# Kernel optimization log

Hardware: AMD Instinct MI355X
Metric: run time of the kernel (lower is better)

## Reference

```python
import jax, jax.numpy as jnp
import numpy as np

BN_EPS = 1e-5

def setup_inputs() -> dict:
    key = jax.random.key(0)
    ks = jax.random.split(key, 6)
    B, C, N = 8, 256, 4096
    da = C // 4
    return {
        "x": jax.random.normal(ks[0], (B, C, N), dtype=jnp.float32),
        "Wq": jax.random.normal(ks[1], (da, C), dtype=jnp.float32) * (C ** -0.5),
        "Wk": jax.random.normal(ks[2], (da, C), dtype=jnp.float32) * (C ** -0.5),
        "Wv": jax.random.normal(ks[3], (C, C), dtype=jnp.float32) * (C ** -0.5),
        "Wp": jax.random.normal(ks[4], (C, C), dtype=jnp.float32) * (C ** -0.5),
        "bn_gamma": jnp.ones((C,), dtype=jnp.float32),
        "bn_beta": jnp.zeros((C,), dtype=jnp.float32),
        "bn_mean": jnp.zeros((C,), dtype=jnp.float32),
        "bn_var": jnp.ones((C,), dtype=jnp.float32),
    }

def reference(x, Wq, Wk, Wv, Wp, bn_gamma, bn_beta, bn_mean, bn_var):
    # x: [B, C, N]; 1x1 Conv1d == channel matmul
    q = jnp.einsum('bcn,dc->bnd', x, Wq)          # [B, N, da]
    k = jnp.einsum('bcn,dc->bdn', x, Wk)          # [B, da, N]
    v = jnp.einsum('bcn,dc->bnd', x, Wv)          # [B, N, C]
    energy = jnp.einsum('bnd,bdm->bnm', q, k)     # [B, N, N]
    # offset-attention double normalization: softmax over dim=1 (rows), then L1 over dim=-1
    attn = jax.nn.softmax(energy, axis=1)
    attn = attn / (1e-9 + attn.sum(axis=-1, keepdims=True))
    fsa = jnp.einsum('bnm,bmc->bcn', attn, v)     # [B, C, N]
    y = x - fsa
    h = jnp.einsum('bcn,dc->bdn', y, Wp)          # 1x1 conv of LBR
    # BatchNorm1d (inference-mode with running stats)
    inv = bn_gamma / jnp.sqrt(bn_var + BN_EPS)
    h = h * inv[None, :, None] + (bn_beta - bn_mean * inv)[None, :, None]
    return jax.nn.relu(h) + x
```

## Files before the change

kernel.cpp:

```cpp
#include <hip/hip_runtime.h>
#include <math.h>

#define BD 8
#define CD 256
#define ND 4096
#define DA 64

typedef __attribute__((ext_vector_type(8))) short short8v;
typedef __attribute__((ext_vector_type(4))) float float4v;

static __device__ __forceinline__ float4v mfma16(short8v a, short8v b, float4v c) {
  return __builtin_amdgcn_mfma_f32_16x16x32_bf16(a, b, c, 0, 0, 0);
}
static __device__ __forceinline__ unsigned short f2bf(float f) {
  union { float f; unsigned int u; } v; v.f = f;
  return (unsigned short)((v.u + 0x7fffu + ((v.u >> 16) & 1u)) >> 16);
}
static __device__ __forceinline__ float bf2f(unsigned short h) {
  union { unsigned int u; float f; } v; v.u = (unsigned int)h << 16;
  return v.f;
}
static __device__ __forceinline__ int sw(int row, int c8) {
  return row * 64 + (((c8) ^ (row & 7)) << 3);
}
typedef const __attribute__((address_space(1))) unsigned int g_u32;
typedef __attribute__((address_space(3))) unsigned int l_u32;
static __device__ __forceinline__ void gld16(const void* g, void* l) {
  __builtin_amdgcn_global_load_lds((g_u32*)g, (l_u32*)l, 16, 0, 0);
}

__global__ __launch_bounds__(256) void k_prep(const float* __restrict__ x,
                                              unsigned short* __restrict__ xTh,
                                              unsigned short* __restrict__ xTl) {
  const int n0 = blockIdx.x * 64, c0 = blockIdx.y * 64, b = blockIdx.z;
  __shared__ float Xs[64][68];
  const int tid = threadIdx.x;
  const int r0 = tid >> 4, col4 = (tid & 15) * 4;
#pragma unroll
  for (int j = 0; j < 4; ++j) {
    int r = r0 + j * 16;
    *(float4*)&Xs[r][col4] =
        *(const float4*)&x[((size_t)(b * CD + c0 + r)) * ND + n0 + col4];
  }
  __syncthreads();
  const int n = tid >> 2, cg = (tid & 3) * 16;
  unsigned short h[16], l[16];
#pragma unroll
  for (int j = 0; j < 16; ++j) {
    float v = Xs[cg + j][n];
    h[j] = f2bf(v);
    l[j] = f2bf(v - bf2f(h[j]));
  }
  size_t o = ((size_t)b * ND + n0 + n) * CD + c0 + cg;
#pragma unroll
  for (int j = 0; j < 4; ++j) {
    *(ushort4*)&xTh[o + j * 4] = *(ushort4*)&h[j * 4];
    *(ushort4*)&xTl[o + j * 4] = *(ushort4*)&l[j * 4];
  }
}

__global__ void k_prepW(const float* __restrict__ Wq, const float* __restrict__ Wk,
                        const float* __restrict__ Wv, const float* __restrict__ Wp,
                        unsigned short* Wch, unsigned short* Wcl,
                        unsigned short* Wph, unsigned short* Wpl) {
  int i = blockIdx.x * 256 + threadIdx.x;
  int row = i >> 6, c4 = (i & 63) * 4;
  const float* src; unsigned short *dh, *dl; int r, drow;
  if (row < 64)       { src = Wq; r = row;       dh = Wch; dl = Wcl; drow = row; }
  else if (row < 128) { src = Wk; r = row - 64;  dh = Wch; dl = Wcl; drow = row; }
  else if (row < 384) { src = Wv; r = row - 128; dh = Wch; dl = Wcl; drow = row; }
  else                { src = Wp; r = row - 384; dh = Wph; dl = Wpl; drow = row - 384; }
  float4 f = *(const float4*)&src[(size_t)r * 256 + c4];
  ushort4 hh, ll;
  hh.x = f2bf(f.x); hh.y = f2bf(f.y); hh.z = f2bf(f.z); hh.w = f2bf(f.w);
  ll.x = f2bf(f.x - bf2f(hh.x)); ll.y = f2bf(f.y - bf2f(hh.y));
  ll.z = f2bf(f.z - bf2f(hh.z)); ll.w = f2bf(f.w - bf2f(hh.w));
  *(ushort4*)&dh[(size_t)drow * 256 + c4] = hh;
  *(ushort4*)&dl[(size_t)drow * 256 + c4] = ll;
}

__global__ __launch_bounds__(512) void k_proj(
    const unsigned short* __restrict__ xTh, const unsigned short* __restrict__ xTl,
    const unsigned short* __restrict__ Wch, const unsigned short* __restrict__ Wcl,
    unsigned short* __restrict__ qh, unsigned short* __restrict__ kh,
    unsigned short* __restrict__ kl, unsigned short* __restrict__ vT) {
  const int n0 = blockIdx.x * 128, b = blockIdx.y;
  const int tid = threadIdx.x, w = tid >> 6, lane = tid & 63, lq = lane & 15,
            quad = lane >> 4;
  __shared__ __align__(16) unsigned short xs[2][2][128][40];
  float4v O[24];
#pragma unroll
  for (int t = 0; t < 24; ++t) O[t] = (float4v){0.f, 0.f, 0.f, 0.f};

  const int srow = tid >> 2, sc4 = tid & 3;
  uint4 rh, rl;
  auto load_slice = [&](int ks) {
    size_t a = ((size_t)b * ND + n0 + srow) * CD + ks * 32 + sc4 * 8;
    rh = *(const uint4*)(xTh + a);
    rl = *(const uint4*)(xTl + a);
  };
  auto write_slice = [&](int buf) {
    *(uint4*)&xs[buf][0][srow][sc4 * 8] = rh;
    *(uint4*)&xs[buf][1][srow][sc4 * 8] = rl;
  };
  load_slice(0); write_slice(0);
#pragma unroll 1
  for (int ks = 0; ks < 8; ++ks) {
    __syncthreads();
    if (ks < 7) load_slice(ks + 1);
    short8v bxh = *(const short8v*)&xs[ks & 1][0][w * 16 + lq][quad * 8];
    short8v bxl = *(const short8v*)&xs[ks & 1][1][w * 16 + lq][quad * 8];
#pragma unroll
    for (int t = 0; t < 24; ++t) {
      size_t a = (size_t)(t * 16 + lq) * CD + ks * 32 + quad * 8;
      short8v awh = *(const short8v*)(Wch + a);
      short8v awl = *(const short8v*)(Wcl + a);
      O[t] = mfma16(awh, bxh, O[t]);
      O[t] = mfma16(awl, bxh, O[t]);
      O[t] = mfma16(awh, bxl, O[t]);
    }
    if (ks < 7) write_slice((ks + 1) & 1);
  }
  const int n = n0 + w * 16 + lq;
#pragma unroll
  for (int t = 0; t < 24; ++t) {
    if (t < 4) {
      ushort4 hh;
      hh.x = f2bf(O[t][0]); hh.y = f2bf(O[t][1]);
      hh.z = f2bf(O[t][2]); hh.w = f2bf(O[t][3]);
      *(ushort4*)&qh[((size_t)b * ND + n) * DA + t * 16 + quad * 4] = hh;
    } else if (t < 8) {
      ushort4 hh, ll;
      hh.x = f2bf(O[t][0]); hh.y = f2bf(O[t][1]);
      hh.z = f2bf(O[t][2]); hh.w = f2bf(O[t][3]);
      ll.x = f2bf(O[t][0] - bf2f(hh.x)); ll.y = f2bf(O[t][1] - bf2f(hh.y));
      ll.z = f2bf(O[t][2] - bf2f(hh.z)); ll.w = f2bf(O[t][3] - bf2f(hh.w));
      size_t o = ((size_t)b * ND + n) * DA + (t - 4) * 16 + quad * 4;
      *(ushort4*)&kh[o] = hh;
      *(ushort4*)&kl[o] = ll;
    } else {
#pragma unroll
      for (int r = 0; r < 4; ++r) {
        int c = (t - 8) * 16 + quad * 4 + r;
        vT[((size_t)b * CD + c) * ND + n] = f2bf(O[t][r]);
      }
    }
  }
}

__global__ __launch_bounds__(512, 4) void k_colsum(
    const unsigned short* __restrict__ qh, const unsigned short* __restrict__ khp,
    const unsigned short* __restrict__ klp, float* __restrict__ Dp) {
  const int bid = blockIdx.x, b = bid & 7, half = (bid >> 3) & 1,
            m0 = (bid >> 4) * 128;
  const int nbase = half * 2048;
  const int tid = threadIdx.x, w = tid >> 6, lane = tid & 63, lq = lane & 15,
            quad = lane >> 4;
  const int mq = w & 3, nh = w >> 2;
  __shared__ __align__(16) unsigned short qbuf[3][4096];
  __shared__ float Cb[128];
  short8v bkh[2][2], bkl[2][2];
#pragma unroll
  for (int sub = 0; sub < 2; ++sub)
#pragma unroll
    for (int k = 0; k < 2; ++k) {
      size_t a = ((size_t)b * ND + m0 + mq * 32 + sub * 16 + lq) * DA + k * 32 + quad * 8;
      bkh[sub][k] = *(const short8v*)(khp + a);
      bkl[sub][k] = *(const short8v*)(klp + a);
    }
  const int srow = w * 8 + (lane >> 3), sck = lane & 7;
  auto stageQ = [&](int it, int qn) {
    const unsigned short* src = qh + ((size_t)b * ND + nbase + it * 64 + srow) * DA +
                                ((sck ^ (srow & 7)) << 3);
    gld16(src, &qbuf[qn][0] + (size_t)w * 512);
  };
  stageQ(0, 0);
  stageQ(1, 1);
  asm volatile("s_waitcnt vmcnt(1)\n\ts_barrier" ::: "memory");
  float cs0 = 0.f, cs1 = 0.f;
  int rc = 0, sc = 2;
#pragma unroll 1
  for (int i = 0; i < 32; ++i) {
    if (i < 30) { stageQ(i + 2, sc); sc = (sc + 1 == 3) ? 0 : sc + 1; }
#pragma unroll
    for (int s = 0; s < 2; ++s) {
      short8v ah[2];
#pragma unroll
      for (int k = 0; k < 2; ++k)
        ah[k] = *(const short8v*)&qbuf[rc][sw(nh * 32 + s * 16 + lq, k * 4 + quad)];
#pragma unroll
      for (int sub = 0; sub < 2; ++sub) {
        float4v acc = {0.f, 0.f, 0.f, 0.f};
#pragma unroll
        for (int k = 0; k < 2; ++k) {
          acc = mfma16(ah[k], bkh[sub][k], acc);
          acc = mfma16(ah[k], bkl[sub][k], acc);
        }
        float e0 = __expf(acc[0]) + __expf(acc[1]) + __expf(acc[2]) + __expf(acc[3]);
        if (sub == 0) cs0 += e0; else cs1 += e0;
      }
    }
    rc = (rc + 1 == 3) ? 0 : rc + 1;
    if (i < 30)
      asm volatile("s_waitcnt vmcnt(1) lgkmcnt(0)\n\ts_barrier" ::: "memory");
    else
      asm volatile("s_waitcnt vmcnt(0) lgkmcnt(0)\n\ts_barrier" ::: "memory");
  }
  cs0 += __shfl_down(cs0, 16); cs0 += __shfl_down(cs0, 32);
  cs1 += __shfl_down(cs1, 16); cs1 += __shfl_down(cs1, 32);
  if (nh == 0 && lane < 16) {
    Cb[mq * 32 + lane] = cs0;
    Cb[mq * 32 + 16 + lane] = cs1;
  }
  __syncthreads();
  if (nh == 1 && lane < 16) {
    float t0 = Cb[mq * 32 + lane] + cs0;
    float t1 = Cb[mq * 32 + 16 + lane] + cs1;
    size_t o = (size_t)half * (BD * ND) + (size_t)b * ND + m0 + mq * 32 + lane;
    Dp[o] = t0;
    Dp[o + 16] = t1;
  }
}

__global__ void k_rcp(const float* __restrict__ Dp, float* __restrict__ Drec) {
  int i = blockIdx.x * 256 + threadIdx.x;
  float4 a = *(const float4*)&Dp[(size_t)i * 4];
  float4 c = *(const float4*)&Dp[(size_t)(BD * ND) + (size_t)i * 4];
  float4 r;
  r.x = 1.f / (a.x + c.x); r.y = 1.f / (a.y + c.y);
  r.z = 1.f / (a.z + c.z); r.w = 1.f / (a.w + c.w);
  *(float4*)&Drec[(size_t)i * 4] = r;
}

__global__ __launch_bounds__(512, 2) void k_attn(
    const unsigned short* __restrict__ qh, const unsigned short* __restrict__ khp,
    const unsigned short* __restrict__ klp, const unsigned short* __restrict__ vT,
    const float* __restrict__ Drec, unsigned short* xhy,
    const unsigned short* __restrict__ xTl) {
  const int bid = blockIdx.x, b = bid & 7, n0 = (bid >> 3) * 128;
  const int tid = threadIdx.x, w = tid >> 6, lane = tid & 63, lq = lane & 15,
            quad = lane >> 4;
  const int nh = w & 1, mt = w >> 1;
  __shared__ __align__(16) unsigned short vbuf[3][16384];
  __shared__ __align__(16) unsigned short Pb[2][8192];
  __shared__ float Sb4[4][128];

  short8v aq[4][2];
#pragma unroll
  for (int s = 0; s < 4; ++s)
#pragma unroll
    for (int k = 0; k < 2; ++k)
      aq[s][k] = *(const short8v*)(qh + ((size_t)b * ND + n0 + nh * 64 + s * 16 + lq) * DA +
                                   k * 32 + quad * 8);
  float4v O[4][4];
#pragma unroll
  for (int ct = 0; ct < 4; ++ct)
#pragma unroll
    for (int s = 0; s < 4; ++s) O[ct][s] = (float4v){0.f, 0.f, 0.f, 0.f};
  float rs[4] = {0.f, 0.f, 0.f, 0.f};

  auto stageV = [&](int mtile, int vn) {
    unsigned short* base = &vbuf[vn][0];
#pragma unroll
    for (int j = 0; j < 4; ++j) {
      int cidx = tid + j * 512;
      int row = cidx >> 3, ckpos = cidx & 7;
      const unsigned short* src =
          vT + ((size_t)b * CD + row) * ND + mtile * 64 + ((ckpos ^ (row & 7)) << 3);
      gld16(src, base + (size_t)(w * 64 + j * 512) * 8);
    }
  };
  short8v kc[4], kn[4];
  auto kload = [&](short8v* dst, int mtile) {
#pragma unroll
    for (int k = 0; k < 2; ++k) {
      size_t a = ((size_t)b * ND + mtile * 64 + mt * 16 + lq) * DA + k * 32 + quad * 8;
      dst[k * 2 + 0] = *(const short8v*)(khp + a);
      dst[k * 2 + 1] = *(const short8v*)(klp + a);
    }
  };
  auto doPV = [&](const unsigned short* Pc, const unsigned short* vc) {
#pragma unroll
    for (int ks = 0; ks < 2; ++ks) {
      short8v ap[4];
#pragma unroll
      for (int s = 0; s < 4; ++s)
        ap[s] = *(const short8v*)&Pc[sw(nh * 64 + s * 16 + lq, ks * 4 + quad)];
#pragma unroll
      for (int ct = 0; ct < 4; ++ct) {
        const int trow = (mt * 4 + ct) * 16 + lq;
        short8v bv = *(const short8v*)&vc[sw(trow, ks * 4 + quad)];
#pragma unroll
        for (int s = 0; s < 4; ++s) O[ct][s] = mfma16(bv, ap[s], O[ct][s]);
      }
    }
  };

  float4 drc4, drn4;
  stageV(0, 0);
  kload(kc, 0);
  drc4 = *(const float4*)&Drec[(size_t)b * ND + mt * 16 + quad * 4];

  int vs = 1, vp = 0;
#pragma unroll 1
  for (int i = 0; i < 64; ++i) {
    if (i > 0) {
      doPV(&Pb[(i - 1) & 1][0], &vbuf[vp][0]);
      vp = (vp + 1 == 3) ? 0 : vp + 1;
    }
    if (i < 63) {
      kload(kn, i + 1);
      drn4 = *(const float4*)&Drec[(size_t)b * ND + (i + 1) * 64 + mt * 16 + quad * 4];
      stageV(i + 1, vs);
      vs = (vs + 1 == 3) ? 0 : vs + 1;
    }
    unsigned short* Pcur = &Pb[i & 1][0];
#pragma unroll
    for (int s = 0; s < 4; ++s) {
      float4v acc = {0.f, 0.f, 0.f, 0.f};
#pragma unroll
      for (int k = 0; k < 2; ++k) {
        acc = mfma16(kc[k * 2 + 0], aq[s][k], acc);
        acc = mfma16(kc[k * 2 + 1], aq[s][k], acc);
      }
      float p0 = __expf(acc[0]) * drc4.x;
      float p1 = __expf(acc[1]) * drc4.y;
      float p2 = __expf(acc[2]) * drc4.z;
      float p3 = __expf(acc[3]) * drc4.w;
      rs[s] += (p0 + p1) + (p2 + p3);
      unsigned int w0 =
          (__float_as_uint(p0) >> 16) | (__float_as_uint(p1) & 0xffff0000u);
      unsigned int w1 =
          (__float_as_uint(p2) >> 16) | (__float_as_uint(p3) & 0xffff0000u);
      const int nl = nh * 64 + s * 16 + lq;
      const int c8 = mt * 2 + (quad >> 1);
      uint2 wv; wv.x = w0; wv.y = w1;
      *(uint2*)&Pcur[nl * 64 + ((c8 ^ (nl & 7)) << 3) + ((quad & 1) << 2)] = wv;
    }
    if (i < 63) {
#pragma unroll
      for (int t = 0; t < 4; ++t) kc[t] = kn[t];
      drc4 = drn4;
    }
    if (i < 63)
      asm volatile("s_waitcnt vmcnt(4) lgkmcnt(0)\n\ts_barrier" ::: "memory");
    else
      asm volatile("s_waitcnt vmcnt(0) lgkmcnt(0)\n\ts_barrier" ::: "memory");
  }
  doPV(&Pb[1][0], &vbuf[vp][0]);

#pragma unroll
  for (int s = 0; s < 4; ++s) {
    rs[s] += __shfl_xor(rs[s], 16);
    rs[s] += __shfl_xor(rs[s], 32);
  }
  if (lane < 16) {
#pragma unroll
    for (int s = 0; s < 4; ++s) Sb4[mt][nh * 64 + s * 16 + lane] = rs[s];
  }
  __syncthreads();
  float rsc[4];
#pragma unroll
  for (int s = 0; s < 4; ++s) {
    const int nloc = nh * 64 + s * 16 + lq;
    rsc[s] = 1.0f / (1e-9f + Sb4[0][nloc] + Sb4[1][nloc] + Sb4[2][nloc] + Sb4[3][nloc]);
  }
#pragma unroll
  for (int ct = 0; ct < 4; ++ct) {
    const int cb = (mt * 4 + ct) * 16 + quad * 4;
#pragma unroll
    for (int s = 0; s < 4; ++s) {
      const int n = n0 + nh * 64 + s * 16 + lq;
      const size_t off = ((size_t)b * ND + n) * CD + cb;
      ushort4 h4 = *(const ushort4*)&xhy[off];
      ushort4 l4 = *(const ushort4*)&xTl[off];
      ushort4 o4;
      o4.x = f2bf(bf2f(h4.x) + bf2f(l4.x) - O[ct][s][0] * rsc[s]);
      o4.y = f2bf(bf2f(h4.y) + bf2f(l4.y) - O[ct][s][1] * rsc[s]);
      o4.z = f2bf(bf2f(h4.z) + bf2f(l4.z) - O[ct][s][2] * rsc[s]);
      o4.w = f2bf(bf2f(h4.w) + bf2f(l4.w) - O[ct][s][3] * rsc[s]);
      *(ushort4*)&xhy[off] = o4;
    }
  }
}

__global__ __launch_bounds__(256) void k_final(const unsigned short* __restrict__ y,
                                               const unsigned short* __restrict__ Wpb,
                                               const float* __restrict__ x,
                                               const float* __restrict__ gamma,
                                               const float* __restrict__ beta,
                                               const float* __restrict__ mean,
                                               const float* __restrict__ var,
                                               float* __restrict__ out) {
  const int bid = blockIdx.x;
  const int b = bid & 7;
  const int rem = bid >> 3;
  const int n0 = (rem & 63) * 64;
  const int d0 = (rem >> 6) * 64;
  const int tid = threadIdx.x;
  const int wave = tid >> 6, lane = tid & 63, lq = lane & 15, quad = lane >> 4;
  const int dw = d0 + wave * 16;
  float4v O[4];
#pragma unroll
  for (int s = 0; s < 4; ++s) O[s] = (float4v){0.f, 0.f, 0.f, 0.f};
#pragma unroll
  for (int chh = 0; chh < 8; ++chh) {
    const size_t ab = (size_t)(dw + lq) * CD + chh * 32 + quad * 8;
    short8v a0 = *(const short8v*)(Wpb + ab);
#pragma unroll
    for (int s = 0; s < 4; ++s) {
      const size_t bb = ((size_t)b * ND + n0 + s * 16 + lq) * CD + chh * 32 + quad * 8;
      short8v bv = *(const short8v*)(y + bb);
      O[s] = mfma16(a0, bv, O[s]);
    }
  }
#pragma unroll
  for (int r = 0; r < 4; ++r) {
    const int d = dw + quad * 4 + r;
    const float inv  = gamma[d] / sqrtf(var[d] + 1e-5f);
    const float bias = beta[d] - mean[d] * inv;
#pragma unroll
    for (int s = 0; s < 4; ++s) {
      const int n = n0 + s * 16 + lq;
      const size_t oi = ((size_t)b * CD + d) * ND + n;
      out[oi] = fmaxf(O[s][r] * inv + bias, 0.f) + x[oi];
    }
  }
}

extern "C" void kernel_launch(void* const* d_in, const int* in_sizes, int n_in,
                              void* d_out, int out_size, void* d_ws, size_t ws_size,
                              hipStream_t stream) {
  const float* x     = (const float*)d_in[0];
  const float* Wq    = (const float*)d_in[1];
  const float* Wk    = (const float*)d_in[2];
  const float* Wv    = (const float*)d_in[3];
  const float* Wp    = (const float*)d_in[4];
  const float* gamma = (const float*)d_in[5];
  const float* beta  = (const float*)d_in[6];
  const float* mean  = (const float*)d_in[7];
  const float* var   = (const float*)d_in[8];
  float* out = (float*)d_out;

  char* wsp = (char*)d_ws;
  unsigned short* qhp = (unsigned short*)wsp; wsp += (size_t)BD * ND * DA * 2;
  unsigned short* khp = (unsigned short*)wsp; wsp += (size_t)BD * ND * DA * 2;
  unsigned short* klp = (unsigned short*)wsp; wsp += (size_t)BD * ND * DA * 2;
  unsigned short* vT  = (unsigned short*)wsp; wsp += (size_t)BD * CD * ND * 2;
  unsigned short* xTh = (unsigned short*)wsp; wsp += (size_t)BD * ND * CD * 2;
  unsigned short* xTl = (unsigned short*)wsp; wsp += (size_t)BD * ND * CD * 2;
  unsigned short* Wch = (unsigned short*)wsp; wsp += (size_t)384 * 256 * 2;
  unsigned short* Wcl = (unsigned short*)wsp; wsp += (size_t)384 * 256 * 2;
  unsigned short* Wph = (unsigned short*)wsp; wsp += (size_t)256 * 256 * 2;
  unsigned short* Wpl = (unsigned short*)wsp; wsp += (size_t)256 * 256 * 2;
  float* Drec = (float*)wsp; wsp += (size_t)BD * ND * 4;
  float* Dp   = (float*)wsp; wsp += (size_t)2 * BD * ND * 4;
  unsigned short* y = xTh;

  dim3 blk(256), blk5(512);
  k_prep<<<dim3(ND / 64, CD / 64, BD), blk, 0, stream>>>(x, xTh, xTl);
  k_prepW<<<dim3(160), blk, 0, stream>>>(Wq, Wk, Wv, Wp, Wch, Wcl, Wph, Wpl);
  k_proj<<<dim3(ND / 128, BD), blk5, 0, stream>>>(xTh, xTl, Wch, Wcl, qhp, khp,
                                                  klp, vT);
  k_colsum<<<dim3(512), blk5, 0, stream>>>(qhp, khp, klp, Dp);
  k_rcp<<<dim3(32), blk, 0, stream>>>(Dp, Drec);
  k_attn<<<dim3(256), blk5, 0, stream>>>(qhp, khp, klp, vT, Drec, y, xTl);
  k_final<<<dim3(2048), blk, 0, stream>>>(y, Wph, x, gamma, beta, mean, var, out);
}
```

Measured before the change: 443.9 us.

## Restructure attention so each wave owns 16 query rows, passing P via bpermute

The attention kernel's work split changes. Before, each wave handled 64 query rows by one m-slice and shared P through LDS. Now each wave owns 16 query rows across all 64 keys of a tile and all 256 output channels. The P tile is moved from the QK accumulator layout into the PV operand layout with ds_bpermute, not through shared memory. This removes the P LDS buffer, the cross-wave row-sum reduction and the split pipeline with one-step-delayed PV. In exchange, every wave reloads all K rows and V reads per tile, holds more accumulators (16 float4), uses only double-buffered V with a full wait each iteration, and loses the QK/PV overlap of the previous schedule.

```diff
diff --git a/kernel.cpp b/kernel.cpp
--- a/kernel.cpp
+++ b/kernel.cpp
@@ -240,24 +240,17 @@
   const int bid = blockIdx.x, b = bid & 7, n0 = (bid >> 3) * 128;
   const int tid = threadIdx.x, w = tid >> 6, lane = tid & 63, lq = lane & 15,
             quad = lane >> 4;
-  const int nh = w & 1, mt = w >> 1;
-  __shared__ __align__(16) unsigned short vbuf[3][16384];
-  __shared__ __align__(16) unsigned short Pb[2][8192];
-  __shared__ float Sb4[4][128];
-
-  short8v aq[4][2];
-#pragma unroll
-  for (int s = 0; s < 4; ++s)
-#pragma unroll
-    for (int k = 0; k < 2; ++k)
-      aq[s][k] = *(const short8v*)(qh + ((size_t)b * ND + n0 + nh * 64 + s * 16 + lq) * DA +
-                                   k * 32 + quad * 8);
-  float4v O[4][4];
-#pragma unroll
-  for (int ct = 0; ct < 4; ++ct)
-#pragma unroll
-    for (int s = 0; s < 4; ++s) O[ct][s] = (float4v){0.f, 0.f, 0.f, 0.f};
-  float rs[4] = {0.f, 0.f, 0.f, 0.f};
+  __shared__ __align__(16) unsigned short vbuf[2][16384];
+
+  short8v aq[2];
+#pragma unroll
+  for (int k = 0; k < 2; ++k)
+    aq[k] = *(const short8v*)(qh + ((size_t)b * ND + n0 + w * 16 + lq) * DA +
+                              k * 32 + quad * 8);
+  float4v O[16];
+#pragma unroll
+  for (int ct = 0; ct < 16; ++ct) O[ct] = (float4v){0.f, 0.f, 0.f, 0.f};
+  float rs = 0.f;
 
   auto stageV = [&](int mtile, int vn) {
     unsigned short* base = &vbuf[vn][0];
@@ -270,117 +263,107 @@
       gld16(src, base + (size_t)(w * 64 + j * 512) * 8);
     }
   };
-  short8v kc[4], kn[4];
-  auto kload = [&](short8v* dst, int mtile) {
-#pragma unroll
-    for (int k = 0; k < 2; ++k) {
-      size_t a = ((size_t)b * ND + mtile * 64 + mt * 16 + lq) * DA + k * 32 + quad * 8;
-      dst[k * 2 + 0] = *(const short8v*)(khp + a);
-      dst[k * 2 + 1] = *(const short8v*)(klp + a);
-    }
-  };
-  auto doPV = [&](const unsigned short* Pc, const unsigned short* vc) {
-#pragma unroll
-    for (int ks = 0; ks < 2; ++ks) {
-      short8v ap[4];
-#pragma unroll
-      for (int s = 0; s < 4; ++s)
-        ap[s] = *(const short8v*)&Pc[sw(nh * 64 + s * 16 + lq, ks * 4 + quad)];
-#pragma unroll
-      for (int ct = 0; ct < 4; ++ct) {
-        const int trow = (mt * 4 + ct) * 16 + lq;
-        short8v bv = *(const short8v*)&vc[sw(trow, ks * 4 + quad)];
-#pragma unroll
-        for (int s = 0; s < 4; ++s) O[ct][s] = mfma16(bv, ap[s], O[ct][s]);
+  short8v kc[4][2][2];
+  auto kload = [&](int mt) {
+#pragma unroll
+    for (int mtile = 0; mtile < 4; ++mtile)
+#pragma unroll
+      for (int k = 0; k < 2; ++k) {
+        size_t a = ((size_t)b * ND + mt * 64 + mtile * 16 + lq) * DA + k * 32 + quad * 8;
+        kc[mtile][k][0] = *(const short8v*)(khp + a);
+        kc[mtile][k][1] = *(const short8v*)(klp + a);
       }
-    }
-  };
-
-  float4 drc4, drn4;
+  };
+  float4 drc[4];
+  auto dload = [&](int mt) {
+#pragma unroll
+    for (int mtile = 0; mtile < 4; ++mtile)
+      drc[mtile] = *(const float4*)&Drec[(size_t)b * ND + mt * 64 + mtile * 16 + quad * 4];
+  };
+  const int bp0 = (lq + ((quad & 1) * 2) * 16) * 4;
+  const int bp1 = bp0 + 64;
+  const bool hi = (quad >> 1) != 0;
+
   stageV(0, 0);
-  kload(kc, 0);
-  drc4 = *(const float4*)&Drec[(size_t)b * ND + mt * 16 + quad * 4];
-
-  int vs = 1, vp = 0;
+  kload(0);
+  dload(0);
+  asm volatile("s_waitcnt vmcnt(0)\n\ts_barrier" ::: "memory");
+
 #pragma unroll 1
   for (int i = 0; i < 64; ++i) {
-    if (i > 0) {
-      doPV(&Pb[(i - 1) & 1][0], &vbuf[vp][0]);
-      vp = (vp + 1 == 3) ? 0 : vp + 1;
-    }
-    if (i < 63) {
-      kload(kn, i + 1);
-      drn4 = *(const float4*)&Drec[(size_t)b * ND + (i + 1) * 64 + mt * 16 + quad * 4];
-      stageV(i + 1, vs);
-      vs = (vs + 1 == 3) ? 0 : vs + 1;
-    }
-    unsigned short* Pcur = &Pb[i & 1][0];
-#pragma unroll
-    for (int s = 0; s < 4; ++s) {
-      float4v acc = {0.f, 0.f, 0.f, 0.f};
+    if (i < 63) stageV(i + 1, (i + 1) & 1);
+    float4v acc[4];
+#pragma unroll
+    for (int mtile = 0; mtile < 4; ++mtile) {
+      acc[mtile] = (float4v){0.f, 0.f, 0.f, 0.f};
 #pragma unroll
       for (int k = 0; k < 2; ++k) {
-        acc = mfma16(kc[k * 2 + 0], aq[s][k], acc);
-        acc = mfma16(kc[k * 2 + 1], aq[s][k], acc);
+        acc[mtile] = mfma16(kc[mtile][k][0], aq[k], acc[mtile]);
+        acc[mtile] = mfma16(kc[mtile][k][1], aq[k], acc[mtile]);
       }
-      float p0 = __expf(acc[0]) * drc4.x;
-      float p1 = __expf(acc[1]) * drc4.y;
-      float p2 = __expf(acc[2]) * drc4.z;
-      float p3 = __expf(acc[3]) * drc4.w;
-      rs[s] += (p0 + p1) + (p2 + p3);
-      unsigned int w0 =
-          (__float_as_uint(p0) >> 16) | (__float_as_uint(p1) & 0xffff0000u);
-      unsigned int w1 =
-          (__float_as_uint(p2) >> 16) | (__float_as_uint(p3) & 0xffff0000u);
-      const int nl = nh * 64 + s * 16 + lq;
-      const int c8 = mt * 2 + (quad >> 1);
-      uint2 wv; wv.x = w0; wv.y = w1;
-      *(uint2*)&Pcur[nl * 64 + ((c8 ^ (nl & 7)) << 3) + ((quad & 1) << 2)] = wv;
-    }
-    if (i < 63) {
-#pragma unroll
-      for (int t = 0; t < 4; ++t) kc[t] = kn[t];
-      drc4 = drn4;
+    }
+    if (i < 63) kload(i + 1);
+    unsigned int w0[4], w1[4];
+#pragma unroll
+    for (int mtile = 0; mtile < 4; ++mtile) {
+      float p0 = __expf(acc[mtile][0]) * drc[mtile].x;
+      float p1 = __expf(acc[mtile][1]) * drc[mtile].y;
+      float p2 = __expf(acc[mtile][2]) * drc[mtile].z;
+      float p3 = __expf(acc[mtile][3]) * drc[mtile].w;
+      rs += (p0 + p1) + (p2 + p3);
+      w0[mtile] = (__float_as_uint(p0) >> 16) | (__float_as_uint(p1) & 0xffff0000u);
+      w1[mtile] = (__float_as_uint(p2) >> 16) | (__float_as_uint(p3) & 0xffff0000u);
+    }
+    if (i < 63) dload(i + 1);
+    short8v ap[2];
+#pragma unroll
+    for (int ks = 0; ks < 2; ++ks) {
+      int a0 = __builtin_amdgcn_ds_bpermute(bp0, (int)w0[2 * ks]);
+      int b0 = __builtin_amdgcn_ds_bpermute(bp0, (int)w1[2 * ks]);
+      int c0 = __builtin_amdgcn_ds_bpermute(bp0, (int)w0[2 * ks + 1]);
+      int d0 = __builtin_amdgcn_ds_bpermute(bp0, (int)w1[2 * ks + 1]);
+      int a1 = __builtin_amdgcn_ds_bpermute(bp1, (int)w0[2 * ks]);
+      int b1 = __builtin_amdgcn_ds_bpermute(bp1, (int)w1[2 * ks]);
+      int c1 = __builtin_amdgcn_ds_bpermute(bp1, (int)w0[2 * ks + 1]);
+      int d1 = __builtin_amdgcn_ds_bpermute(bp1, (int)w1[2 * ks + 1]);
+      uint4 u;
+      u.x = (unsigned int)(hi ? c0 : a0);
+      u.y = (unsigned int)(hi ? d0 : b0);
+      u.z = (unsigned int)(hi ? c1 : a1);
+      u.w = (unsigned int)(hi ? d1 : b1);
+      union { uint4 u4; short8v s8; } cvt; cvt.u4 = u;
+      ap[ks] = cvt.s8;
+    }
+    const unsigned short* vc = &vbuf[i & 1][0];
+#pragma unroll
+    for (int ct = 0; ct < 16; ++ct) {
+      const int trow = ct * 16 + lq;
+#pragma unroll
+      for (int ks = 0; ks < 2; ++ks) {
+        short8v bv = *(const short8v*)&vc[sw(trow, ks * 4 + quad)];
+        O[ct] = mfma16(bv, ap[ks], O[ct]);
+      }
     }
     if (i < 63)
-      asm volatile("s_waitcnt vmcnt(4) lgkmcnt(0)\n\ts_barrier" ::: "memory");
-    else
       asm volatile("s_waitcnt vmcnt(0) lgkmcnt(0)\n\ts_barrier" ::: "memory");
   }
-  doPV(&Pb[1][0], &vbuf[vp][0]);
-
-#pragma unroll
-  for (int s = 0; s < 4; ++s) {
-    rs[s] += __shfl_xor(rs[s], 16);
-    rs[s] += __shfl_xor(rs[s], 32);
-  }
-  if (lane < 16) {
-#pragma unroll
-    for (int s = 0; s < 4; ++s) Sb4[mt][nh * 64 + s * 16 + lane] = rs[s];
-  }
-  __syncthreads();
-  float rsc[4];
-#pragma unroll
-  for (int s = 0; s < 4; ++s) {
-    const int nloc = nh * 64 + s * 16 + lq;
-    rsc[s] = 1.0f / (1e-9f + Sb4[0][nloc] + Sb4[1][nloc] + Sb4[2][nloc] + Sb4[3][nloc]);
-  }
-#pragma unroll
-  for (int ct = 0; ct < 4; ++ct) {
-    const int cb = (mt * 4 + ct) * 16 + quad * 4;
-#pragma unroll
-    for (int s = 0; s < 4; ++s) {
-      const int n = n0 + nh * 64 + s * 16 + lq;
-      const size_t off = ((size_t)b * ND + n) * CD + cb;
-      ushort4 h4 = *(const ushort4*)&xhy[off];
-      ushort4 l4 = *(const ushort4*)&xTl[off];
-      ushort4 o4;
-      o4.x = f2bf(bf2f(h4.x) + bf2f(l4.x) - O[ct][s][0] * rsc[s]);
-      o4.y = f2bf(bf2f(h4.y) + bf2f(l4.y) - O[ct][s][1] * rsc[s]);
-      o4.z = f2bf(bf2f(h4.z) + bf2f(l4.z) - O[ct][s][2] * rsc[s]);
-      o4.w = f2bf(bf2f(h4.w) + bf2f(l4.w) - O[ct][s][3] * rsc[s]);
-      *(ushort4*)&xhy[off] = o4;
-    }
+
+  rs += __shfl_xor(rs, 16);
+  rs += __shfl_xor(rs, 32);
+  const float rsc = 1.0f / (1e-9f + rs);
+  const int n = n0 + w * 16 + lq;
+#pragma unroll
+  for (int ct = 0; ct < 16; ++ct) {
+    const int cb = ct * 16 + quad * 4;
+    const size_t off = ((size_t)b * ND + n) * CD + cb;
+    ushort4 h4 = *(const ushort4*)&xhy[off];
+    ushort4 l4 = *(const ushort4*)&xTl[off];
+    ushort4 o4;
+    o4.x = f2bf(bf2f(h4.x) + bf2f(l4.x) - O[ct][0] * rsc);
+    o4.y = f2bf(bf2f(h4.y) + bf2f(l4.y) - O[ct][1] * rsc);
+    o4.z = f2bf(bf2f(h4.z) + bf2f(l4.z) - O[ct][2] * rsc);
+    o4.w = f2bf(bf2f(h4.w) + bf2f(l4.w) - O[ct][3] * rsc);
+    *(ushort4*)&xhy[off] = o4;
   }
 }
 
```

Result: slower. 592.4 us (+33.4%).

## Rewrite attention kernel with 32x32 MFMA and register-resident P, removing LDS P buffer

Applied to the files above, without the earlier changes.

The attention kernel moves from 16x16x32 bf16 MFMA tiles to 32x32x16 tiles. Each wave now computes a 32x32 energy block and feeds the exponentiated probabilities straight into the PV MFMA as B operands after a cross-half lane shuffle, so the P tile no longer round-trips through shared memory. The work split changes so that two waves share each n-range over different halves of m. Their partial O accumulators are reduced through LDS scratch at the end, which adds extra barriers, more accumulator registers and an epilogue reduction.

```diff
diff --git a/kernel.cpp b/kernel.cpp
--- a/kernel.cpp
+++ b/kernel.cpp
@@ -8,9 +8,13 @@
 
 typedef __attribute__((ext_vector_type(8))) short short8v;
 typedef __attribute__((ext_vector_type(4))) float float4v;
+typedef __attribute__((ext_vector_type(16))) float f32x16;
 
 static __device__ __forceinline__ float4v mfma16(short8v a, short8v b, float4v c) {
   return __builtin_amdgcn_mfma_f32_16x16x32_bf16(a, b, c, 0, 0, 0);
+}
+static __device__ __forceinline__ f32x16 mfma32(short8v a, short8v b, f32x16 c) {
+  return __builtin_amdgcn_mfma_f32_32x32x16_bf16(a, b, c, 0, 0, 0);
 }
 static __device__ __forceinline__ unsigned short f2bf(float f) {
   union { float f; unsigned int u; } v; v.f = f;
@@ -238,148 +242,178 @@
     const float* __restrict__ Drec, unsigned short* xhy,
     const unsigned short* __restrict__ xTl) {
   const int bid = blockIdx.x, b = bid & 7, n0 = (bid >> 3) * 128;
-  const int tid = threadIdx.x, w = tid >> 6, lane = tid & 63, lq = lane & 15,
-            quad = lane >> 4;
-  const int nh = w & 1, mt = w >> 1;
+  const int tid = threadIdx.x, w = tid >> 6, lane = tid & 63;
+  const int l32 = lane & 31, hi = lane >> 5;
+  const int mh = w & 1, nq = w >> 1;
   __shared__ __align__(16) unsigned short vbuf[3][16384];
-  __shared__ __align__(16) unsigned short Pb[2][8192];
-  __shared__ float Sb4[4][128];
-
-  short8v aq[4][2];
-#pragma unroll
-  for (int s = 0; s < 4; ++s)
-#pragma unroll
-    for (int k = 0; k < 2; ++k)
-      aq[s][k] = *(const short8v*)(qh + ((size_t)b * ND + n0 + nh * 64 + s * 16 + lq) * DA +
-                                   k * 32 + quad * 8);
-  float4v O[4][4];
-#pragma unroll
-  for (int ct = 0; ct < 4; ++ct)
-#pragma unroll
-    for (int s = 0; s < 4; ++s) O[ct][s] = (float4v){0.f, 0.f, 0.f, 0.f};
-  float rs[4] = {0.f, 0.f, 0.f, 0.f};
-
-  auto stageV = [&](int mtile, int vn) {
+  __shared__ float Sb[2][128];
+
+  short8v aq[4];
+#pragma unroll
+  for (int kk = 0; kk < 4; ++kk)
+    aq[kk] = *(const short8v*)(qh + ((size_t)b * ND + n0 + nq * 32 + l32) * DA +
+                               kk * 16 + hi * 8);
+  f32x16 O[8];
+  const f32x16 z16 = {0.f, 0.f, 0.f, 0.f, 0.f, 0.f, 0.f, 0.f,
+                      0.f, 0.f, 0.f, 0.f, 0.f, 0.f, 0.f, 0.f};
+#pragma unroll
+  for (int ct = 0; ct < 8; ++ct) O[ct] = z16;
+  float rs = 0.f;
+
+  auto stageV = [&](int mt, int vn) {
     unsigned short* base = &vbuf[vn][0];
 #pragma unroll
     for (int j = 0; j < 4; ++j) {
       int cidx = tid + j * 512;
       int row = cidx >> 3, ckpos = cidx & 7;
       const unsigned short* src =
-          vT + ((size_t)b * CD + row) * ND + mtile * 64 + ((ckpos ^ (row & 7)) << 3);
+          vT + ((size_t)b * CD + row) * ND + mt * 64 + ((ckpos ^ (row & 7)) << 3);
       gld16(src, base + (size_t)(w * 64 + j * 512) * 8);
     }
   };
-  short8v kc[4], kn[4];
-  auto kload = [&](short8v* dst, int mtile) {
-#pragma unroll
-    for (int k = 0; k < 2; ++k) {
-      size_t a = ((size_t)b * ND + mtile * 64 + mt * 16 + lq) * DA + k * 32 + quad * 8;
-      dst[k * 2 + 0] = *(const short8v*)(khp + a);
-      dst[k * 2 + 1] = *(const short8v*)(klp + a);
-    }
-  };
-  auto doPV = [&](const unsigned short* Pc, const unsigned short* vc) {
-#pragma unroll
-    for (int ks = 0; ks < 2; ++ks) {
-      short8v ap[4];
-#pragma unroll
-      for (int s = 0; s < 4; ++s)
-        ap[s] = *(const short8v*)&Pc[sw(nh * 64 + s * 16 + lq, ks * 4 + quad)];
-#pragma unroll
-      for (int ct = 0; ct < 4; ++ct) {
-        const int trow = (mt * 4 + ct) * 16 + lq;
-        short8v bv = *(const short8v*)&vc[sw(trow, ks * 4 + quad)];
-#pragma unroll
-        for (int s = 0; s < 4; ++s) O[ct][s] = mfma16(bv, ap[s], O[ct][s]);
+  short8v kc[4][2];
+  auto kload = [&](int mt) {
+#pragma unroll
+    for (int kk = 0; kk < 4; ++kk) {
+      size_t a = ((size_t)b * ND + mt * 64 + mh * 32 + l32) * DA + kk * 16 + hi * 8;
+      kc[kk][0] = *(const short8v*)(khp + a);
+      kc[kk][1] = *(const short8v*)(klp + a);
+    }
+  };
+  float dr[16];
+  auto dload = [&](int mt) {
+#pragma unroll
+    for (int g = 0; g < 4; ++g) {
+      float4 t = *(const float4*)&Drec[(size_t)b * ND + mt * 64 + mh * 32 +
+                                       g * 8 + hi * 4];
+      dr[g * 4 + 0] = t.x; dr[g * 4 + 1] = t.y;
+      dr[g * 4 + 2] = t.z; dr[g * 4 + 3] = t.w;
+    }
+  };
+  short8v pf[2];
+  auto doPV = [&](const unsigned short* vc) {
+#pragma unroll
+    for (int ct = 0; ct < 8; ++ct) {
+      const int row = ct * 32 + l32;
+#pragma unroll
+      for (int kk2 = 0; kk2 < 2; ++kk2) {
+        short8v bv = *(const short8v*)&vc[sw(row, mh * 4 + kk2 * 2 + hi)];
+        O[ct] = mfma32(bv, pf[kk2], O[ct]);
       }
     }
   };
 
-  float4 drc4, drn4;
   stageV(0, 0);
-  kload(kc, 0);
-  drc4 = *(const float4*)&Drec[(size_t)b * ND + mt * 16 + quad * 4];
+  kload(0);
+  dload(0);
 
   int vs = 1, vp = 0;
 #pragma unroll 1
   for (int i = 0; i < 64; ++i) {
     if (i > 0) {
-      doPV(&Pb[(i - 1) & 1][0], &vbuf[vp][0]);
+      doPV(&vbuf[vp][0]);
       vp = (vp + 1 == 3) ? 0 : vp + 1;
     }
+    f32x16 acc = z16;
+#pragma unroll
+    for (int kk = 0; kk < 4; ++kk) {
+      acc = mfma32(kc[kk][0], aq[kk], acc);
+      acc = mfma32(kc[kk][1], aq[kk], acc);
+    }
+    unsigned int pw[8];
+#pragma unroll
+    for (int j = 0; j < 8; ++j) {
+      float pa = __expf(acc[2 * j]) * dr[2 * j];
+      float pb = __expf(acc[2 * j + 1]) * dr[2 * j + 1];
+      rs += pa + pb;
+      pw[j] = (__float_as_uint(pa) >> 16) | (__float_as_uint(pb) & 0xffff0000u);
+    }
+    {
+      unsigned int xw[8];
+#pragma unroll
+      for (int j = 0; j < 8; ++j) xw[j] = (unsigned int)__shfl_xor((int)pw[j], 32);
+      uint4 u0, u1;
+      u0.x = hi ? xw[2] : pw[0]; u0.y = hi ? xw[3] : pw[1];
+      u0.z = hi ? pw[2] : xw[0]; u0.w = hi ? pw[3] : xw[1];
+      u1.x = hi ? xw[6] : pw[4]; u1.y = hi ? xw[7] : pw[5];
+      u1.z = hi ? pw[6] : xw[4]; u1.w = hi ? pw[7] : xw[5];
+      union { uint4 u4; short8v s8; } c0, c1;
+      c0.u4 = u0; c1.u4 = u1;
+      pf[0] = c0.s8;
+      pf[1] = c1.s8;
+    }
     if (i < 63) {
-      kload(kn, i + 1);
-      drn4 = *(const float4*)&Drec[(size_t)b * ND + (i + 1) * 64 + mt * 16 + quad * 4];
+      kload(i + 1);
+      dload(i + 1);
       stageV(i + 1, vs);
       vs = (vs + 1 == 3) ? 0 : vs + 1;
-    }
-    unsigned short* Pcur = &Pb[i & 1][0];
-#pragma unroll
-    for (int s = 0; s < 4; ++s) {
-      float4v acc = {0.f, 0.f, 0.f, 0.f};
-#pragma unroll
-      for (int k = 0; k < 2; ++k) {
-        acc = mfma16(kc[k * 2 + 0], aq[s][k], acc);
-        acc = mfma16(kc[k * 2 + 1], aq[s][k], acc);
-      }
-      float p0 = __expf(acc[0]) * drc4.x;
-      float p1 = __expf(acc[1]) * drc4.y;
-      float p2 = __expf(acc[2]) * drc4.z;
-      float p3 = __expf(acc[3]) * drc4.w;
-      rs[s] += (p0 + p1) + (p2 + p3);
-      unsigned int w0 =
-          (__float_as_uint(p0) >> 16) | (__float_as_uint(p1) & 0xffff0000u);
-      unsigned int w1 =
-          (__float_as_uint(p2) >> 16) | (__float_as_uint(p3) & 0xffff0000u);
-      const int nl = nh * 64 + s * 16 + lq;
-      const int c8 = mt * 2 + (quad >> 1);
-      uint2 wv; wv.x = w0; wv.y = w1;
-      *(uint2*)&Pcur[nl * 64 + ((c8 ^ (nl & 7)) << 3) + ((quad & 1) << 2)] = wv;
-    }
-    if (i < 63) {
-#pragma unroll
-      for (int t = 0; t < 4; ++t) kc[t] = kn[t];
-      drc4 = drn4;
     }
     if (i < 63)
       asm volatile("s_waitcnt vmcnt(4) lgkmcnt(0)\n\ts_barrier" ::: "memory");
     else
       asm volatile("s_waitcnt vmcnt(0) lgkmcnt(0)\n\ts_barrier" ::: "memory");
   }
-  doPV(&Pb[1][0], &vbuf[vp][0]);
-
-#pragma unroll
-  for (int s = 0; s < 4; ++s) {
-    rs[s] += __shfl_xor(rs[s], 16);
-    rs[s] += __shfl_xor(rs[s], 32);
-  }
-  if (lane < 16) {
-#pragma unroll
-    for (int s = 0; s < 4; ++s) Sb4[mt][nh * 64 + s * 16 + lane] = rs[s];
-  }
+  doPV(&vbuf[vp][0]);
+
+  rs += __shfl_xor(rs, 32);
+  if (lane < 32) Sb[mh][nq * 32 + lane] = rs;
+
+  float* scratch = (float*)&vbuf[0][0];
   __syncthreads();
-  float rsc[4];
-#pragma unroll
-  for (int s = 0; s < 4; ++s) {
-    const int nloc = nh * 64 + s * 16 + lq;
-    rsc[s] = 1.0f / (1e-9f + Sb4[0][nloc] + Sb4[1][nloc] + Sb4[2][nloc] + Sb4[3][nloc]);
-  }
-#pragma unroll
-  for (int ct = 0; ct < 4; ++ct) {
-    const int cb = (mt * 4 + ct) * 16 + quad * 4;
-#pragma unroll
-    for (int s = 0; s < 4; ++s) {
-      const int n = n0 + nh * 64 + s * 16 + lq;
-      const size_t off = ((size_t)b * ND + n) * CD + cb;
-      ushort4 h4 = *(const ushort4*)&xhy[off];
-      ushort4 l4 = *(const ushort4*)&xTl[off];
-      ushort4 o4;
-      o4.x = f2bf(bf2f(h4.x) + bf2f(l4.x) - O[ct][s][0] * rsc[s]);
-      o4.y = f2bf(bf2f(h4.y) + bf2f(l4.y) - O[ct][s][1] * rsc[s]);
-      o4.z = f2bf(bf2f(h4.z) + bf2f(l4.z) - O[ct][s][2] * rsc[s]);
-      o4.w = f2bf(bf2f(h4.w) + bf2f(l4.w) - O[ct][s][3] * rsc[s]);
-      *(ushort4*)&xhy[off] = o4;
+#pragma unroll
+  for (int half = 0; half < 2; ++half) {
+    if (mh == 1) {
+#pragma unroll
+      for (int ct = 0; ct < 4; ++ct) {
+        const int idx = ((nq * 4 + ct) * 64 + lane) * 16;
+#pragma unroll
+        for (int g = 0; g < 4; ++g) {
+          float4 t;
+          t.x = O[half * 4 + ct][g * 4 + 0];
+          t.y = O[half * 4 + ct][g * 4 + 1];
+          t.z = O[half * 4 + ct][g * 4 + 2];
+          t.w = O[half * 4 + ct][g * 4 + 3];
+          *(float4*)&scratch[idx + g * 4] = t;
+        }
+      }
+    }
+    __syncthreads();
+    if (mh == 0) {
+#pragma unroll
+      for (int ct = 0; ct < 4; ++ct) {
+        const int idx = ((nq * 4 + ct) * 64 + lane) * 16;
+#pragma unroll
+        for (int g = 0; g < 4; ++g) {
+          float4 t = *(const float4*)&scratch[idx + g * 4];
+          O[half * 4 + ct][g * 4 + 0] += t.x;
+          O[half * 4 + ct][g * 4 + 1] += t.y;
+          O[half * 4 + ct][g * 4 + 2] += t.z;
+          O[half * 4 + ct][g * 4 + 3] += t.w;
+        }
+      }
+    }
+    __syncthreads();
+  }
+
+  const int nl = nq * 32 + l32;
+  const float rsc = 1.0f / (1e-9f + Sb[0][nl] + Sb[1][nl]);
+  if (mh == 0) {
+    const int n = n0 + nq * 32 + l32;
+#pragma unroll
+    for (int ct = 0; ct < 8; ++ct) {
+#pragma unroll
+      for (int g = 0; g < 4; ++g) {
+        const int cb = ct * 32 + g * 8 + hi * 4;
+        const size_t off = ((size_t)b * ND + n) * CD + cb;
+        ushort4 h4 = *(const ushort4*)&xhy[off];
+        ushort4 l4 = *(const ushort4*)&xTl[off];
+        ushort4 o4;
+        o4.x = f2bf(bf2f(h4.x) + bf2f(l4.x) - O[ct][g * 4 + 0] * rsc);
+        o4.y = f2bf(bf2f(h4.y) + bf2f(l4.y) - O[ct][g * 4 + 1] * rsc);
+        o4.z = f2bf(bf2f(h4.z) + bf2f(l4.z) - O[ct][g * 4 + 2] * rsc);
+        o4.w = f2bf(bf2f(h4.w) + bf2f(l4.w) - O[ct][g * 4 + 3] * rsc);
+        *(ushort4*)&xhy[off] = o4;
+      }
     }
   }
 }
```

Result: slower. 510.2 us (+14.9%).
